# Optimization experiments

Measured on AMD Instinct MI355X. Metric: run time of the kernel, lower is better.

## Reference

```python
import jax, jax.numpy as jnp
import numpy as np

CROP = 7          # crop_size from init_kwargs
OFFSET = 0.5      # sample_offset from init_kwargs
MIN_LEVEL = 2     # smallest pyramid level key


def _multilevel_roi_align(feats, boxes):
    """Faithful port of spatial_transform_ops.multilevel_crop_and_resize.

    feats: list of [B, H_l, W_l, C] arrays, levels MIN_LEVEL..MIN_LEVEL+len-1.
    boxes: [B, N, 4] un-normalized [y1, x1, y2, x2].
    returns [B, N, CROP, CROP, C].
    """
    B, N, _ = boxes.shape
    C = feats[0].shape[-1]
    heights = [f.shape[1] for f in feats]
    widths = [f.shape[2] for f in feats]
    max_level = MIN_LEVEL + len(feats) - 1

    # Flatten all levels into one [B, sum(H_l*W_l), C] buffer (like features_r2).
    flat = jnp.concatenate([f.reshape(B, -1, C) for f in feats], axis=1)
    dim_sizes = np.array([h * w for h, w in zip(heights, widths)], np.int64)
    lvl_offsets = jnp.asarray(
        np.concatenate([[0], np.cumsum(dim_sizes)[:-1]]).astype(np.int32))
    lvl_widths = jnp.asarray(np.array(widths, np.int32))

    # --- level assignment: floor(log2(sqrt(h*w)/224)) + 4, clipped ---
    bh = boxes[..., 2] - boxes[..., 0]
    bw = boxes[..., 3] - boxes[..., 1]
    areas_sqrt = jnp.sqrt(bh * bw)
    lev_f = jnp.floor(jnp.log2(areas_sqrt / 224.0)) + 4.0
    lev = jnp.clip(lev_f, MIN_LEVEL, max_level).astype(jnp.int32)   # [B,N]

    # project boxes to assigned level
    scale = jnp.exp2(lev.astype(boxes.dtype))
    y0b = boxes[..., 0] / scale
    x0b = boxes[..., 1] / scale
    bh = bh / scale
    bw = bw / scale

    lev0 = lev - MIN_LEVEL
    stride = jnp.exp2(lev0.astype(boxes.dtype))
    bnd_y = jnp.asarray(float(heights[0]), boxes.dtype) / stride - 1.0  # [B,N]
    bnd_x = jnp.asarray(float(widths[0]), boxes.dtype) / stride - 1.0

    # --- compute_grid_positions ---
    i = jnp.arange(CROP, dtype=boxes.dtype)
    gy = y0b[..., None] + (i + OFFSET) * bh[..., None] / CROP   # [B,N,S]
    gx = x0b[..., None] + (i + OFFSET) * bw[..., None] / CROP
    y0 = jnp.minimum(jnp.maximum(jnp.floor(gy), 0.0), bnd_y[..., None])
    y1 = jnp.minimum(y0 + 1.0, bnd_y[..., None])
    x0 = jnp.minimum(jnp.maximum(jnp.floor(gx), 0.0), bnd_x[..., None])
    x1 = jnp.minimum(x0 + 1.0, bnd_x[..., None])
    ly = gy - y0
    lx = gx - x0
    ky = jnp.stack([1.0 - ly, ly], axis=-1)   # [B,N,S,2]
    kx = jnp.stack([1.0 - lx, lx], axis=-1)
    yi = jnp.stack([y0, y1], axis=-1).astype(jnp.int32)  # [B,N,S,2]
    xi = jnp.stack([x0, x1], axis=-1).astype(jnp.int32)

    # --- flattened gather indices (level offset + y*W_l + x) ---
    w_l = lvl_widths[lev0]        # [B,N]
    off_l = lvl_offsets[lev0]     # [B,N]
    idx = (off_l[:, :, None, None, None, None]
           + (yi * w_l[..., None, None])[:, :, :, :, None, None]
           + xi[:, :, None, None, :, :])            # [B,N,S,2,S,2]
    g = jax.vmap(lambda f, ix: f[ix])(flat, idx.reshape(B, -1))
    g = g.reshape(B, N, CROP, 2, CROP, 2, C)

    # --- bilinear interpolation (kernel*4 then 2x2 avg_pool == weighted sum) ---
    return jnp.einsum('bnpiqjc,bnpi,bnqj->bnpqc', g, ky, kx)


def setup_inputs() -> dict:
    key = jax.random.key(0)
    kf2, kf3, kf4, kf5, kyx, khw = jax.random.split(key, 6)
    B, N, C = 8, 256, 256
    feat2 = jax.random.normal(kf2, (B, 256, 256, C), jnp.float32)
    feat3 = jax.random.normal(kf3, (B, 128, 128, C), jnp.float32)
    feat4 = jax.random.normal(kf4, (B, 64, 64, C), jnp.float32)
    feat5 = jax.random.normal(kf5, (B, 32, 32, C), jnp.float32)
    # valid [y1,x1,y2,x2] boxes in a 1024x1024 image, sizes spanning all levels
    yx = jax.random.uniform(kyx, (B, N, 2), jnp.float32, 0.0, 512.0)
    hw = jax.random.uniform(khw, (B, N, 2), jnp.float32, 16.0, 512.0)
    boxes = jnp.concatenate([yx, yx + hw], axis=-1)
    return {"feat2": feat2, "feat3": feat3, "feat4": feat4,
            "feat5": feat5, "boxes": boxes}


def reference(feat2, feat3, feat4, feat5, boxes):
    return _multilevel_roi_align([feat2, feat3, feat4, feat5], boxes)
```

## Files before the change

### kernel.cpp

```cpp
#include <hip/hip_runtime.h>


#define CROPS 7
#define NCH   256
#define NBOX  256

__global__ __launch_bounds__(64)
void roi_align_kernel(const float* __restrict__ f2,
                      const float* __restrict__ f3,
                      const float* __restrict__ f4,
                      const float* __restrict__ f5,
                      const float* __restrict__ boxes,
                      float* __restrict__ out)
{
    const int blk = blockIdx.x;
    const int pq  = blk % 49;
    const int bn  = blk / 49;
    const int p   = pq / 7;
    const int q   = pq - p * 7;
    const int b   = bn >> 8;

    const float* bx = boxes + (size_t)bn * 4;
    const float by1 = bx[0], bx1 = bx[1], by2 = bx[2], bx2 = bx[3];
    float bh = by2 - by1;
    float bw = bx2 - bx1;

    const float as   = sqrtf(bh * bw);
    float levf = floorf(log2f(as / 224.0f)) + 4.0f;
    levf = fminf(fmaxf(levf, 2.0f), 5.0f);
    const int   lev   = (int)levf;
    const float scale = exp2f(levf);

    const float y0b = by1 / scale;
    const float x0b = bx1 / scale;
    const float bhp = bh / scale;
    const float bwp = bw / scale;

    const int   lev0 = lev - 2;
    const int   W    = 256 >> lev0;
    const float bnd  = (float)(W - 1);

    const float gy = y0b + ((float)p + 0.5f) * bhp / 7.0f;
    const float gx = x0b + ((float)q + 0.5f) * bwp / 7.0f;

    const float fy0 = fminf(fmaxf(floorf(gy), 0.0f), bnd);
    const float fy1 = fminf(fy0 + 1.0f, bnd);
    const float fx0 = fminf(fmaxf(floorf(gx), 0.0f), bnd);
    const float fx1 = fminf(fx0 + 1.0f, bnd);

    const float ly = gy - fy0;
    const float lx = gx - fx0;
    const float ky0 = 1.0f - ly, ky1 = ly;
    const float kx0 = 1.0f - lx, kx1 = lx;

    const int yi0 = (int)fy0, yi1 = (int)fy1;
    const int xi0 = (int)fx0, xi1 = (int)fx1;

    const float* base;
    if      (lev0 == 0) base = f2 + (size_t)b * (256u * 256u * NCH);
    else if (lev0 == 1) base = f3 + (size_t)b * (128u * 128u * NCH);
    else if (lev0 == 2) base = f4 + (size_t)b * ( 64u *  64u * NCH);
    else                base = f5 + (size_t)b * ( 32u *  32u * NCH);

    const int t = threadIdx.x;

    const float4* r00 = (const float4*)(base + ((size_t)yi0 * W + xi0) * NCH) + t;
    const float4* r01 = (const float4*)(base + ((size_t)yi0 * W + xi1) * NCH) + t;
    const float4* r10 = (const float4*)(base + ((size_t)yi1 * W + xi0) * NCH) + t;
    const float4* r11 = (const float4*)(base + ((size_t)yi1 * W + xi1) * NCH) + t;

    const float4 v00 = *r00;
    const float4 v01 = *r01;
    const float4 v10 = *r10;
    const float4 v11 = *r11;

    const float w00 = ky0 * kx0;
    const float w01 = ky0 * kx1;
    const float w10 = ky1 * kx0;
    const float w11 = ky1 * kx1;

    float4 o;
    o.x = v00.x * w00 + v01.x * w01 + v10.x * w10 + v11.x * w11;
    o.y = v00.y * w00 + v01.y * w01 + v10.y * w10 + v11.y * w11;
    o.z = v00.z * w00 + v01.z * w01 + v10.z * w10 + v11.z * w11;
    o.w = v00.w * w00 + v01.w * w01 + v10.w * w10 + v11.w * w11;

    float4* op = (float4*)(out + (size_t)blk * NCH) + t;
    *op = o;
}

extern "C" void kernel_launch(void* const* d_in, const int* in_sizes, int n_in,
                              void* d_out, int out_size, void* d_ws, size_t ws_size,
                              hipStream_t stream) {
    const float* f2    = (const float*)d_in[0];
    const float* f3    = (const float*)d_in[1];
    const float* f4    = (const float*)d_in[2];
    const float* f5    = (const float*)d_in[3];
    const float* boxes = (const float*)d_in[4];
    float* out = (float*)d_out;

    const int nblocks = 8 * NBOX * 49;
    roi_align_kernel<<<nblocks, 64, 0, stream>>>(f2, f3, f4, f5, boxes, out);
}
```

Baseline: 694.8 us.

## Assign one box per block and process two crop points per wave iteration

After: 702.6 us. Within noise of the previous version (+1.1%).

```diff
diff --git a/kernel.cpp b/kernel.cpp
--- a/kernel.cpp
+++ b/kernel.cpp
@@ -1,11 +1,12 @@
 #include <hip/hip_runtime.h>
 
 
-#define CROPS 7
-#define NCH   256
-#define NBOX  256
+typedef float v4f __attribute__((ext_vector_type(4)));
 
-__global__ __launch_bounds__(64)
+#define NCH  256
+#define NBOX 256
+
+__global__ __launch_bounds__(256)
 void roi_align_kernel(const float* __restrict__ f2,
                       const float* __restrict__ f3,
                       const float* __restrict__ f4,
@@ -13,48 +14,27 @@
                       const float* __restrict__ boxes,
                       float* __restrict__ out)
 {
-    const int blk = blockIdx.x;
-    const int pq  = blk % 49;
-    const int bn  = blk / 49;
-    const int p   = pq / 7;
-    const int q   = pq - p * 7;
-    const int b   = bn >> 8;
+    const int bn = blockIdx.x;
+    const int b  = bn >> 8;
 
     const float* bx = boxes + (size_t)bn * 4;
-    const float by1 = bx[0], bx1 = bx[1], by2 = bx[2], bx2 = bx[3];
-    float bh = by2 - by1;
-    float bw = bx2 - bx1;
+    const float by1 = bx[0], bx1v = bx[1], by2 = bx[2], bx2v = bx[3];
+    const float bh = by2 - by1;
+    const float bw = bx2v - bx1v;
 
-    const float as   = sqrtf(bh * bw);
+    const float as = sqrtf(bh * bw);
     float levf = floorf(log2f(as / 224.0f)) + 4.0f;
     levf = fminf(fmaxf(levf, 2.0f), 5.0f);
-    const int   lev   = (int)levf;
     const float scale = exp2f(levf);
+    const int   lev0  = (int)levf - 2;
 
     const float y0b = by1 / scale;
-    const float x0b = bx1 / scale;
+    const float x0b = bx1v / scale;
     const float bhp = bh / scale;
     const float bwp = bw / scale;
 
-    const int   lev0 = lev - 2;
-    const int   W    = 256 >> lev0;
-    const float bnd  = (float)(W - 1);
-
-    const float gy = y0b + ((float)p + 0.5f) * bhp / 7.0f;
-    const float gx = x0b + ((float)q + 0.5f) * bwp / 7.0f;
-
-    const float fy0 = fminf(fmaxf(floorf(gy), 0.0f), bnd);
-    const float fy1 = fminf(fy0 + 1.0f, bnd);
-    const float fx0 = fminf(fmaxf(floorf(gx), 0.0f), bnd);
-    const float fx1 = fminf(fx0 + 1.0f, bnd);
-
-    const float ly = gy - fy0;
-    const float lx = gx - fx0;
-    const float ky0 = 1.0f - ly, ky1 = ly;
-    const float kx0 = 1.0f - lx, kx1 = lx;
-
-    const int yi0 = (int)fy0, yi1 = (int)fy1;
-    const int xi0 = (int)fx0, xi1 = (int)fx1;
+    const int   W   = 256 >> lev0;
+    const float bnd = (float)(W - 1);
 
     const float* base;
     if      (lev0 == 0) base = f2 + (size_t)b * (256u * 256u * NCH);
@@ -62,31 +42,54 @@
     else if (lev0 == 2) base = f4 + (size_t)b * ( 64u *  64u * NCH);
     else                base = f5 + (size_t)b * ( 32u *  32u * NCH);
 
-    const int t = threadIdx.x;
+    const int wv = threadIdx.x >> 6;
+    const int t  = threadIdx.x & 63;
 
-    const float4* r00 = (const float4*)(base + ((size_t)yi0 * W + xi0) * NCH) + t;
-    const float4* r01 = (const float4*)(base + ((size_t)yi0 * W + xi1) * NCH) + t;
-    const float4* r10 = (const float4*)(base + ((size_t)yi1 * W + xi0) * NCH) + t;
-    const float4* r11 = (const float4*)(base + ((size_t)yi1 * W + xi1) * NCH) + t;
+    float* outbn = out + (size_t)bn * 49 * NCH;
 
-    const float4 v00 = *r00;
-    const float4 v01 = *r01;
-    const float4 v10 = *r10;
-    const float4 v11 = *r11;
+    auto corners = [&](int k,
+                       const v4f*& r00, const v4f*& r01,
+                       const v4f*& r10, const v4f*& r11,
+                       float& w00, float& w01, float& w10, float& w11) {
+        const int p = k / 7;
+        const int q = k - p * 7;
+        const float gy = y0b + ((float)p + 0.5f) * bhp / 7.0f;
+        const float gx = x0b + ((float)q + 0.5f) * bwp / 7.0f;
+        const float fy0 = fminf(fmaxf(floorf(gy), 0.0f), bnd);
+        const float fy1 = fminf(fy0 + 1.0f, bnd);
+        const float fx0 = fminf(fmaxf(floorf(gx), 0.0f), bnd);
+        const float fx1 = fminf(fx0 + 1.0f, bnd);
+        const float ly = gy - fy0, lx = gx - fx0;
+        const float ky0 = 1.0f - ly, kx0 = 1.0f - lx;
+        const int yi0 = (int)fy0, yi1 = (int)fy1;
+        const int xi0 = (int)fx0, xi1 = (int)fx1;
+        r00 = (const v4f*)(base + (size_t)(yi0 * W + xi0) * NCH) + t;
+        r01 = (const v4f*)(base + (size_t)(yi0 * W + xi1) * NCH) + t;
+        r10 = (const v4f*)(base + (size_t)(yi1 * W + xi0) * NCH) + t;
+        r11 = (const v4f*)(base + (size_t)(yi1 * W + xi1) * NCH) + t;
+        w00 = ky0 * kx0; w01 = ky0 * lx; w10 = ly * kx0; w11 = ly * lx;
+    };
 
-    const float w00 = ky0 * kx0;
-    const float w01 = ky0 * kx1;
-    const float w10 = ky1 * kx0;
-    const float w11 = ky1 * kx1;
+    for (int k = wv; k < 49; k += 8) {
+        const v4f *a00, *a01, *a10, *a11, *c00, *c01, *c10, *c11;
+        float aw00, aw01, aw10, aw11, cw00, cw01, cw10, cw11;
 
-    float4 o;
-    o.x = v00.x * w00 + v01.x * w01 + v10.x * w10 + v11.x * w11;
-    o.y = v00.y * w00 + v01.y * w01 + v10.y * w10 + v11.y * w11;
-    o.z = v00.z * w00 + v01.z * w01 + v10.z * w10 + v11.z * w11;
-    o.w = v00.w * w00 + v01.w * w01 + v10.w * w10 + v11.w * w11;
+        corners(k, a00, a01, a10, a11, aw00, aw01, aw10, aw11);
+        const bool two = (k + 4) < 49;
+        const int  k2  = two ? k + 4 : k;
+        corners(k2, c00, c01, c10, c11, cw00, cw01, cw10, cw11);
 
-    float4* op = (float4*)(out + (size_t)blk * NCH) + t;
-    *op = o;
+        const v4f va00 = *a00, va01 = *a01, va10 = *a10, va11 = *a11;
+        const v4f vc00 = *c00, vc01 = *c01, vc10 = *c10, vc11 = *c11;
+
+        v4f oa = va00 * aw00 + va01 * aw01 + va10 * aw10 + va11 * aw11;
+        __builtin_nontemporal_store(oa, (v4f*)(outbn + (size_t)k * NCH) + t);
+
+        if (two) {
+            v4f oc = vc00 * cw00 + vc01 * cw01 + vc10 * cw10 + vc11 * cw11;
+            __builtin_nontemporal_store(oc, (v4f*)(outbn + (size_t)k2 * NCH) + t);
+        }
+    }
 }
 
 extern "C" void kernel_launch(void* const* d_in, const int* in_sizes, int n_in,
@@ -99,6 +102,6 @@
     const float* boxes = (const float*)d_in[4];
     float* out = (float*)d_out;
 
-    const int nblocks = 8 * NBOX * 49;
-    roi_align_kernel<<<nblocks, 64, 0, stream>>>(f2, f3, f4, f5, boxes, out);
+    const int nblocks = 8 * NBOX;
+    roi_align_kernel<<<nblocks, 256, 0, stream>>>(f2, f3, f4, f5, boxes, out);
 }
```
